# Kernel tuning notes

Hardware: AMD Instinct MI355X
Metric: run time of the kernel (lower is better)

Reference implementation:

```python
import jax, jax.numpy as jnp
import numpy as np

NUM_OBJ = 3
MIN_OBJ_SCALE = 0.1
MAX_OBJ_SCALE = 0.8
MIN_Y_SCALE = 0.75
MAX_Y_SCALE = 1.25
OBJ_POS_BOUND = 0.9
EPS_FIX = 0.095
BIG = 1e12


def setup_inputs() -> dict:
    key = jax.random.key(0)
    k1, k2, k3 = jax.random.split(key, 3)
    n, T, C, H, W = 64, 32, 3, 64, 64
    x = jax.random.normal(k1, (n, T, C, H, W), dtype=jnp.float32)
    d = C * H * W
    W_enc = jax.random.normal(k2, (d, NUM_OBJ * 8), dtype=jnp.float32) / np.sqrt(d).astype(np.float32)
    b_enc = jax.random.normal(k3, (NUM_OBJ * 8,), dtype=jnp.float32) * 0.01
    return {"x": x, "W_enc": W_enc, "b_enc": b_enc}


def _constrain_zp_mean(zp):
    # zp: (nTo, 8) -> mean (nTo, 4). std branch is discarded by forward().
    zm = jnp.concatenate([jax.nn.sigmoid(zp[:, 0:2]), 2.0 * jax.nn.sigmoid(zp[:, 2:4]) - 1.0], -1)
    set_max = jnp.array([[MAX_OBJ_SCALE - MIN_OBJ_SCALE, MAX_Y_SCALE - MIN_Y_SCALE, OBJ_POS_BOUND, OBJ_POS_BOUND]], dtype=zp.dtype)
    set_min = jnp.array([[MIN_OBJ_SCALE, MIN_Y_SCALE, 0.0, 0.0]], dtype=zp.dtype)
    return zm * set_max + set_min


def _greedy_assign(errors):
    # errors: (n, o, o). Greedy row-by-row argmin, masking out used columns with BIG,
    # exactly as the torch fault-fix loop does via scatter of 1e12.
    n, o, _ = errors.shape
    def step(used, i):
        e = errors[:, i, :] + used * BIG
        j = jnp.argmin(e, -1)
        used = used + jax.nn.one_hot(j, o, dtype=errors.dtype)
        return used, j
    _, js = jax.lax.scan(step, jnp.zeros((n, o), errors.dtype), jnp.arange(o))
    return jnp.moveaxis(js, 0, 1)  # (n, o)


def _match_objects(z):
    # z: (n, T, o, 4). Sequential greedy matching over time.
    def step(prev, z_t):
        curr = jax.lax.stop_gradient(z_t[:, :, 2:4])          # (n, o, 2)
        prv = jax.lax.stop_gradient(prev[:, :, 2:4])          # (n, o, 2)
        errors = jnp.sum((prv[:, :, None, :] - curr[:, None, :, :]) ** 2, -1)  # (n, i, j)
        idx = jnp.argmin(errors, -1)                          # (n, o)
        # fault = assignment is not a permutation (num_obj==3 check from source)
        ok = jnp.all(idx[:, 1:] != idx[:, :-1], -1) & (idx[:, 0] != idx[:, 2])
        gidx = _greedy_assign(errors)
        idx = jnp.where(ok[:, None], idx, gidx)
        match = jnp.take_along_axis(z_t, idx[:, :, None], axis=1)
        return match, match
    z0 = z[:, 0]
    _, rest = jax.lax.scan(step, z0, jnp.moveaxis(z[:, 1:], 1, 0))
    return jnp.concatenate([z0[:, None], jnp.moveaxis(rest, 0, 1)], 1)


def _fix_supair(z):
    # z: (n, T, o, 4). Replace isolated position jumps with neighbor average.
    n, T, o, d = z.shape
    diffs = jax.lax.stop_gradient(jnp.abs(z[:, 1:, :, :2] - z[:, :-1, :, :2]))
    zpad2 = jnp.zeros((n, 1, o, 2), z.dtype)
    prev = jnp.concatenate([zpad2, diffs], 1)
    after = jnp.concatenate([diffs, zpad2], 1)
    mask = (prev > EPS_FIX) & (after > EPS_FIX)               # (n, T, o, 2)
    zpad = jnp.zeros((n, 1, o, d), z.dtype)
    smooth = jnp.concatenate([zpad, (z[:, :-2] + z[:, 2:]) / 2, zpad], 1)
    mask_full = jnp.concatenate((d // 2) * [mask], -1)        # (n, T, o, 4)
    return jnp.where(mask_full, smooth, z)


def reference(x, W_enc, b_enc):
    n, T = x.shape[0], x.shape[1]
    # encoder: per-frame linear to (num_obj, 8) z-parameters
    zp = x.reshape(n * T, -1) @ W_enc + b_enc                  # (nT, o*8)
    zm = _constrain_zp_mean(zp.reshape(-1, 8))                 # (nTo, 4)
    z = zm.reshape(n, T, NUM_OBJ, 4)
    z = _match_objects(z)
    z = _fix_supair(z)
    # v_from_state
    v = z[:, 1:, :, 2:] - z[:, :-1, :, 2:]
    zf = jnp.concatenate([z[:, 1:], v], -1)                    # (n, T-1, o, 6)
    zf = jnp.concatenate([jnp.zeros_like(zf[:, 0:1]), zf], 1)  # (n, T, o, 6)
    zf = zf[:, 1:, :, 2:]                                      # (n, T-1, o, 4)
    zf = jnp.concatenate([(zf[..., :2] + 1) / 2 * 10, zf[..., 2:] / 2 * 10], -1)
    zf = jnp.concatenate([zf[..., :2] / 5, zf[..., 2:] * 2], -1)
    return zf
```

## Files before the change

kernel.cpp:

```cpp
#include <hip/hip_runtime.h>

#define N_B   64
#define T_S   32
#define DIM   12288
#define ROWS  2048
#define NCOL  12
#define RPB   16
#define KSPL  8
#define KSEG  (DIM / KSPL)
#define JSTEP (KSEG / 256)

__global__ __launch_bounds__(256) void k_tw(const float* __restrict__ W,
                                            float* __restrict__ Wt) {
    const int idx = blockIdx.x * 256 + threadIdx.x;
    const int c   = idx / DIM;
    const int k   = idx - c * DIM;
    const int cm  = ((c >> 2) << 3) | (c & 3);
    Wt[idx] = W[k * 24 + cm];
}

__global__ __launch_bounds__(256) void k_gemm(const float* __restrict__ x,
                                              const float* __restrict__ Wt,
                                              float* __restrict__ part) {
    const int rb   = blockIdx.x >> 3;
    const int sg   = blockIdx.x & 7;
    const int tid  = threadIdx.x;
    const int wave = tid >> 6;
    const int lane = tid & 63;
    const int r0   = rb * RPB + wave * 4;
    const int kb0  = sg * KSEG + lane * 4;

    float acc[4][NCOL];
#pragma unroll
    for (int r = 0; r < 4; ++r)
#pragma unroll
        for (int c = 0; c < NCOL; ++c) acc[r][c] = 0.f;

#pragma unroll 1
    for (int j = 0; j < JSTEP; ++j) {
        const int kb = kb0 + j * 256;
        float4 wv[NCOL];
#pragma unroll
        for (int c = 0; c < NCOL; ++c)
            wv[c] = *(const float4*)(Wt + (size_t)c * DIM + kb);
        float4 xv[4];
#pragma unroll
        for (int r = 0; r < 4; ++r)
            xv[r] = *(const float4*)(x + (size_t)(r0 + r) * DIM + kb);
#pragma unroll
        for (int r = 0; r < 4; ++r)
#pragma unroll
            for (int c = 0; c < NCOL; ++c)
                acc[r][c] += xv[r].x * wv[c].x + xv[r].y * wv[c].y +
                             xv[r].z * wv[c].z + xv[r].w * wv[c].w;
    }

#pragma unroll
    for (int r = 0; r < 4; ++r)
#pragma unroll
        for (int c = 0; c < NCOL; ++c) {
            float v = acc[r][c];
            v += __shfl_xor(v, 32, 64);
            v += __shfl_xor(v, 16, 64);
            v += __shfl_xor(v, 8, 64);
            v += __shfl_xor(v, 4, 64);
            v += __shfl_xor(v, 2, 64);
            v += __shfl_xor(v, 1, 64);
            acc[r][c] = v;
        }

    __shared__ float red[RPB * NCOL];
    if (lane == 0) {
#pragma unroll
        for (int r = 0; r < 4; ++r)
#pragma unroll
            for (int c = 0; c < NCOL; ++c)
                red[(wave * 4 + r) * NCOL + c] = acc[r][c];
    }
    __syncthreads();

    if (tid < RPB * NCOL)
        part[(size_t)sg * (ROWS * NCOL) + (size_t)rb * (RPB * NCOL) + tid] = red[tid];
}

__global__ __launch_bounds__(256) void k_reduce(const float* __restrict__ part,
                                                const float* __restrict__ b_enc,
                                                float* __restrict__ zbuf) {
    const int rc = blockIdx.x * 256 + threadIdx.x;
    float s = 0.f;
#pragma unroll
    for (int i = 0; i < KSPL; ++i) s += part[(size_t)i * (ROWS * NCOL) + rc];

    const int c  = rc % NCOL;
    const int o  = c >> 2;
    const int cp = c & 3;
    s += b_enc[o * 8 + cp];
    const float sg = 1.f / (1.f + expf(-s));
    float v;
    if (cp == 0)      v = sg * 0.7f + 0.1f;
    else if (cp == 1) v = sg * 0.5f + 0.75f;
    else              v = (2.f * sg - 1.f) * 0.9f;
    zbuf[rc] = v;
}

__global__ __launch_bounds__(64) void k_post(const float* __restrict__ zbuf,
                                             float* __restrict__ out) {
    __shared__ float z[T_S * NCOL];
    __shared__ float zm[T_S * NCOL];
    __shared__ float zf[T_S * NCOL];
    __shared__ int   perm[T_S];
    const int b   = blockIdx.x;
    const int tid = threadIdx.x;

#pragma unroll
    for (int i = 0; i < 6; ++i)
        z[tid + 64 * i] = zbuf[b * 384 + tid + 64 * i];
    __syncthreads();

    if (tid == 0) {
        float px0 = z[2],  py0 = z[3];
        float px1 = z[6],  py1 = z[7];
        float px2 = z[10], py2 = z[11];
        for (int t = 1; t < T_S; ++t) {
            const int base = t * 12;
            const float cx0 = z[base + 2],  cy0 = z[base + 3];
            const float cx1 = z[base + 6],  cy1 = z[base + 7];
            const float cx2 = z[base + 10], cy2 = z[base + 11];

            float dx, dy;
            dx = px0 - cx0; dy = py0 - cy0; const float e00 = dx * dx + dy * dy;
            dx = px0 - cx1; dy = py0 - cy1; const float e01 = dx * dx + dy * dy;
            dx = px0 - cx2; dy = py0 - cy2; const float e02 = dx * dx + dy * dy;
            dx = px1 - cx0; dy = py1 - cy0; const float e10 = dx * dx + dy * dy;
            dx = px1 - cx1; dy = py1 - cy1; const float e11 = dx * dx + dy * dy;
            dx = px1 - cx2; dy = py1 - cy2; const float e12 = dx * dx + dy * dy;
            dx = px2 - cx0; dy = py2 - cy0; const float e20 = dx * dx + dy * dy;
            dx = px2 - cx1; dy = py2 - cy1; const float e21 = dx * dx + dy * dy;
            dx = px2 - cx2; dy = py2 - cy2; const float e22 = dx * dx + dy * dy;

            auto amin3 = [](float a0, float a1, float a2) {
                int j = 0; float e = a0;
                if (a1 < e) { e = a1; j = 1; }
                if (a2 < e) { j = 2; }
                return j;
            };
            int i0 = amin3(e00, e01, e02);
            int i1 = amin3(e10, e11, e12);
            int i2 = amin3(e20, e21, e22);
            const bool ok = (i1 != i0) && (i2 != i1) && (i0 != i2);
            if (!ok) {
                float u0 = 0.f, u1 = 0.f, u2 = 0.f;
                i0 = amin3(e00, e01, e02);
                if (i0 == 0) u0 = 1.f; else if (i0 == 1) u1 = 1.f; else u2 = 1.f;
                i1 = amin3(e10 + u0 * 1e12f, e11 + u1 * 1e12f, e12 + u2 * 1e12f);
                if (i1 == 0) u0 = 1.f; else if (i1 == 1) u1 = 1.f; else u2 = 1.f;
                i2 = amin3(e20 + u0 * 1e12f, e21 + u1 * 1e12f, e22 + u2 * 1e12f);
            }
            perm[t] = i0 * 9 + i1 * 3 + i2;
            px0 = (i0 == 0) ? cx0 : (i0 == 1) ? cx1 : cx2;
            py0 = (i0 == 0) ? cy0 : (i0 == 1) ? cy1 : cy2;
            px1 = (i1 == 0) ? cx0 : (i1 == 1) ? cx1 : cx2;
            py1 = (i1 == 0) ? cy0 : (i1 == 1) ? cy1 : cy2;
            px2 = (i2 == 0) ? cx0 : (i2 == 1) ? cx1 : cx2;
            py2 = (i2 == 0) ? cy0 : (i2 == 1) ? cy1 : cy2;
        }
    }
    __syncthreads();

#pragma unroll
    for (int ii = 0; ii < 6; ++ii) {
        const int i  = tid + 64 * ii;
        const int t  = i / 12;
        const int j  = i - t * 12;
        const int k  = j >> 2;
        const int ch = j & 3;
        int p = k;
        if (t > 0) {
            const int code = perm[t];
            p = (k == 0) ? code / 9 : (k == 1) ? (code % 9) / 3 : code % 3;
        }
        zm[i] = z[t * 12 + p * 4 + ch];
    }
    __syncthreads();

#pragma unroll
    for (int ii = 0; ii < 6; ++ii) {
        const int i  = tid + 64 * ii;
        const int t  = i / 12;
        const int j  = i - t * 12;
        const int o  = j >> 2;
        const int cc = j & 1;
        const int mb = o * 4 + cc;
        const float pd = (t >= 1)  ? fabsf(zm[t * 12 + mb] - zm[(t - 1) * 12 + mb]) : 0.f;
        const float ad = (t <= 30) ? fabsf(zm[(t + 1) * 12 + mb] - zm[t * 12 + mb]) : 0.f;
        const bool  m  = (pd > 0.095f) && (ad > 0.095f);
        const float sm = (t >= 1 && t <= 30)
                             ? (zm[(t - 1) * 12 + j] + zm[(t + 1) * 12 + j]) * 0.5f
                             : 0.f;
        zf[i] = m ? sm : zm[t * 12 + j];
    }
    __syncthreads();

    for (int i = tid; i < 31 * 12; i += 64) {
        const int t  = i / 12;
        const int j  = i - t * 12;
        const int o  = j >> 2;
        const int c2 = j & 3;
        const int pb = o * 4 + 2 + (c2 & 1);
        float v;
        if (c2 < 2) v = zf[(t + 1) * 12 + pb] + 1.f;
        else        v = (zf[(t + 1) * 12 + pb] - zf[t * 12 + pb]) * 10.f;
        out[b * 372 + i] = v;
    }
}

extern "C" void kernel_launch(void* const* d_in, const int* in_sizes, int n_in,
                              void* d_out, int out_size, void* d_ws, size_t ws_size,
                              hipStream_t stream) {
    (void)in_sizes; (void)n_in; (void)out_size; (void)ws_size;
    const float* x     = (const float*)d_in[0];
    const float* W_enc = (const float*)d_in[1];
    const float* b_enc = (const float*)d_in[2];
    float* out  = (float*)d_out;

    float* zbuf = (float*)d_ws;
    float* Wt   = zbuf + ROWS * NCOL;
    float* part = Wt + NCOL * DIM;

    k_tw    <<<(NCOL * DIM) / 256, 256, 0, stream>>>(W_enc, Wt);
    k_gemm  <<<(ROWS / RPB) * KSPL, 256, 0, stream>>>(x, Wt, part);
    k_reduce<<<(ROWS * NCOL) / 256, 256, 0, stream>>>(part, b_enc, zbuf);
    k_post  <<<N_B, 64, 0, stream>>>(zbuf, out);
}
```

Baseline: 174.1 us.

## Double rows per wave in GEMM and split matching into a batch-parallel kernel

Each wave now handles 8 rows instead of 4, so every Wt load is reused across twice as many rows and the GEMM grid is halved. The greedy matching moves out of the single-thread-per-block post kernel into a dedicated kernel where one thread per batch runs the sequential scan over a time-major position buffer written by the reduce kernel. The greedy fallback is now computed branchlessly every step. This adds one more kernel launch and raises register pressure in the GEMM, which may lower occupancy.

```diff
diff --git a/kernel.cpp b/kernel.cpp
--- a/kernel.cpp
+++ b/kernel.cpp
@@ -5,7 +5,9 @@
 #define DIM   12288
 #define ROWS  2048
 #define NCOL  12
-#define RPB   16
+#define RPW   8
+#define WAVES 4
+#define RPB   (RPW * WAVES)
 #define KSPL  8
 #define KSEG  (DIM / KSPL)
 #define JSTEP (KSEG / 256)
@@ -27,36 +29,34 @@
     const int tid  = threadIdx.x;
     const int wave = tid >> 6;
     const int lane = tid & 63;
-    const int r0   = rb * RPB + wave * 4;
+    const int r0   = rb * RPB + wave * RPW;
     const int kb0  = sg * KSEG + lane * 4;
 
-    float acc[4][NCOL];
-#pragma unroll
-    for (int r = 0; r < 4; ++r)
+    float acc[RPW][NCOL];
+#pragma unroll
+    for (int r = 0; r < RPW; ++r)
 #pragma unroll
         for (int c = 0; c < NCOL; ++c) acc[r][c] = 0.f;
 
 #pragma unroll 1
     for (int j = 0; j < JSTEP; ++j) {
         const int kb = kb0 + j * 256;
-        float4 wv[NCOL];
-#pragma unroll
-        for (int c = 0; c < NCOL; ++c)
-            wv[c] = *(const float4*)(Wt + (size_t)c * DIM + kb);
-        float4 xv[4];
-#pragma unroll
-        for (int r = 0; r < 4; ++r)
+        float4 xv[RPW];
+#pragma unroll
+        for (int r = 0; r < RPW; ++r)
             xv[r] = *(const float4*)(x + (size_t)(r0 + r) * DIM + kb);
 #pragma unroll
-        for (int r = 0; r < 4; ++r)
-#pragma unroll
-            for (int c = 0; c < NCOL; ++c)
-                acc[r][c] += xv[r].x * wv[c].x + xv[r].y * wv[c].y +
-                             xv[r].z * wv[c].z + xv[r].w * wv[c].w;
-    }
-
-#pragma unroll
-    for (int r = 0; r < 4; ++r)
+        for (int c = 0; c < NCOL; ++c) {
+            const float4 wv = *(const float4*)(Wt + (size_t)c * DIM + kb);
+#pragma unroll
+            for (int r = 0; r < RPW; ++r)
+                acc[r][c] += xv[r].x * wv.x + xv[r].y * wv.y +
+                             xv[r].z * wv.z + xv[r].w * wv.w;
+        }
+    }
+
+#pragma unroll
+    for (int r = 0; r < RPW; ++r)
 #pragma unroll
         for (int c = 0; c < NCOL; ++c) {
             float v = acc[r][c];
@@ -72,28 +72,31 @@
     __shared__ float red[RPB * NCOL];
     if (lane == 0) {
 #pragma unroll
-        for (int r = 0; r < 4; ++r)
+        for (int r = 0; r < RPW; ++r)
 #pragma unroll
             for (int c = 0; c < NCOL; ++c)
-                red[(wave * 4 + r) * NCOL + c] = acc[r][c];
-    }
-    __syncthreads();
-
-    if (tid < RPB * NCOL)
-        part[(size_t)sg * (ROWS * NCOL) + (size_t)rb * (RPB * NCOL) + tid] = red[tid];
+                red[(wave * RPW + r) * NCOL + c] = acc[r][c];
+    }
+    __syncthreads();
+
+#pragma unroll
+    for (int i = tid; i < RPB * NCOL; i += 256)
+        part[(size_t)sg * (ROWS * NCOL) + (size_t)rb * (RPB * NCOL) + i] = red[i];
 }
 
 __global__ __launch_bounds__(256) void k_reduce(const float* __restrict__ part,
                                                 const float* __restrict__ b_enc,
-                                                float* __restrict__ zbuf) {
+                                                float* __restrict__ zbuf,
+                                                float* __restrict__ zmatch) {
     const int rc = blockIdx.x * 256 + threadIdx.x;
     float s = 0.f;
 #pragma unroll
     for (int i = 0; i < KSPL; ++i) s += part[(size_t)i * (ROWS * NCOL) + rc];
 
-    const int c  = rc % NCOL;
-    const int o  = c >> 2;
-    const int cp = c & 3;
+    const int row = rc / NCOL;
+    const int c   = rc - row * NCOL;
+    const int o   = c >> 2;
+    const int cp  = c & 3;
     s += b_enc[o * 8 + cp];
     const float sg = 1.f / (1.f + expf(-s));
     float v;
@@ -101,10 +104,75 @@
     else if (cp == 1) v = sg * 0.5f + 0.75f;
     else              v = (2.f * sg - 1.f) * 0.9f;
     zbuf[rc] = v;
-}
-
-__global__ __launch_bounds__(64) void k_post(const float* __restrict__ zbuf,
-                                             float* __restrict__ out) {
+
+    if (cp >= 2) {
+        const int b = row >> 5;
+        const int t = row & 31;
+        zmatch[((size_t)t * 64 + b) * 6 + o * 2 + (cp - 2)] = v;
+    }
+}
+
+__global__ __launch_bounds__(64) void k_match(const float* __restrict__ zmatch,
+                                              int* __restrict__ codes) {
+    const int b = threadIdx.x;
+
+    float px0 = zmatch[b * 6 + 0], py0 = zmatch[b * 6 + 1];
+    float px1 = zmatch[b * 6 + 2], py1 = zmatch[b * 6 + 3];
+    float px2 = zmatch[b * 6 + 4], py2 = zmatch[b * 6 + 5];
+
+    auto amin3 = [](float a0, float a1, float a2) {
+        int j = 0; float e = a0;
+        if (a1 < e) { e = a1; j = 1; }
+        if (a2 < e) { j = 2; }
+        return j;
+    };
+
+    for (int t = 1; t < T_S; ++t) {
+        const float* p = zmatch + ((size_t)t * 64 + b) * 6;
+        const float cx0 = p[0], cy0 = p[1];
+        const float cx1 = p[2], cy1 = p[3];
+        const float cx2 = p[4], cy2 = p[5];
+
+        float dx, dy;
+        dx = px0 - cx0; dy = py0 - cy0; const float e00 = dx * dx + dy * dy;
+        dx = px0 - cx1; dy = py0 - cy1; const float e01 = dx * dx + dy * dy;
+        dx = px0 - cx2; dy = py0 - cy2; const float e02 = dx * dx + dy * dy;
+        dx = px1 - cx0; dy = py1 - cy0; const float e10 = dx * dx + dy * dy;
+        dx = px1 - cx1; dy = py1 - cy1; const float e11 = dx * dx + dy * dy;
+        dx = px1 - cx2; dy = py1 - cy2; const float e12 = dx * dx + dy * dy;
+        dx = px2 - cx0; dy = py2 - cy0; const float e20 = dx * dx + dy * dy;
+        dx = px2 - cx1; dy = py2 - cy1; const float e21 = dx * dx + dy * dy;
+        dx = px2 - cx2; dy = py2 - cy2; const float e22 = dx * dx + dy * dy;
+
+        const int i0 = amin3(e00, e01, e02);
+        const int i1 = amin3(e10, e11, e12);
+        const int i2 = amin3(e20, e21, e22);
+
+        float u0 = (i0 == 0) ? 1e12f : 0.f;
+        float u1 = (i0 == 1) ? 1e12f : 0.f;
+        float u2 = (i0 == 2) ? 1e12f : 0.f;
+        const int g1 = amin3(e10 + u0, e11 + u1, e12 + u2);
+        if (g1 == 0) u0 = 1e12f; else if (g1 == 1) u1 = 1e12f; else u2 = 1e12f;
+        const int g2 = amin3(e20 + u0, e21 + u1, e22 + u2);
+
+        const bool ok = (i1 != i0) && (i2 != i1) && (i0 != i2);
+        const int f1 = ok ? i1 : g1;
+        const int f2 = ok ? i2 : g2;
+
+        codes[t * 64 + b] = i0 * 9 + f1 * 3 + f2;
+
+        px0 = (i0 == 0) ? cx0 : (i0 == 1) ? cx1 : cx2;
+        py0 = (i0 == 0) ? cy0 : (i0 == 1) ? cy1 : cy2;
+        px1 = (f1 == 0) ? cx0 : (f1 == 1) ? cx1 : cx2;
+        py1 = (f1 == 0) ? cy0 : (f1 == 1) ? cy1 : cy2;
+        px2 = (f2 == 0) ? cx0 : (f2 == 1) ? cx1 : cx2;
+        py2 = (f2 == 0) ? cy0 : (f2 == 1) ? cy1 : cy2;
+    }
+}
+
+__global__ __launch_bounds__(64) void k_apply(const float* __restrict__ zbuf,
+                                              const int* __restrict__ codes,
+                                              float* __restrict__ out) {
     __shared__ float z[T_S * NCOL];
     __shared__ float zm[T_S * NCOL];
     __shared__ float zf[T_S * NCOL];
@@ -115,56 +183,7 @@
 #pragma unroll
     for (int i = 0; i < 6; ++i)
         z[tid + 64 * i] = zbuf[b * 384 + tid + 64 * i];
-    __syncthreads();
-
-    if (tid == 0) {
-        float px0 = z[2],  py0 = z[3];
-        float px1 = z[6],  py1 = z[7];
-        float px2 = z[10], py2 = z[11];
-        for (int t = 1; t < T_S; ++t) {
-            const int base = t * 12;
-            const float cx0 = z[base + 2],  cy0 = z[base + 3];
-            const float cx1 = z[base + 6],  cy1 = z[base + 7];
-            const float cx2 = z[base + 10], cy2 = z[base + 11];
-
-            float dx, dy;
-            dx = px0 - cx0; dy = py0 - cy0; const float e00 = dx * dx + dy * dy;
-            dx = px0 - cx1; dy = py0 - cy1; const float e01 = dx * dx + dy * dy;
-            dx = px0 - cx2; dy = py0 - cy2; const float e02 = dx * dx + dy * dy;
-            dx = px1 - cx0; dy = py1 - cy0; const float e10 = dx * dx + dy * dy;
-            dx = px1 - cx1; dy = py1 - cy1; const float e11 = dx * dx + dy * dy;
-            dx = px1 - cx2; dy = py1 - cy2; const float e12 = dx * dx + dy * dy;
-            dx = px2 - cx0; dy = py2 - cy0; const float e20 = dx * dx + dy * dy;
-            dx = px2 - cx1; dy = py2 - cy1; const float e21 = dx * dx + dy * dy;
-            dx = px2 - cx2; dy = py2 - cy2; const float e22 = dx * dx + dy * dy;
-
-            auto amin3 = [](float a0, float a1, float a2) {
-                int j = 0; float e = a0;
-                if (a1 < e) { e = a1; j = 1; }
-                if (a2 < e) { j = 2; }
-                return j;
-            };
-            int i0 = amin3(e00, e01, e02);
-            int i1 = amin3(e10, e11, e12);
-            int i2 = amin3(e20, e21, e22);
-            const bool ok = (i1 != i0) && (i2 != i1) && (i0 != i2);
-            if (!ok) {
-                float u0 = 0.f, u1 = 0.f, u2 = 0.f;
-                i0 = amin3(e00, e01, e02);
-                if (i0 == 0) u0 = 1.f; else if (i0 == 1) u1 = 1.f; else u2 = 1.f;
-                i1 = amin3(e10 + u0 * 1e12f, e11 + u1 * 1e12f, e12 + u2 * 1e12f);
-                if (i1 == 0) u0 = 1.f; else if (i1 == 1) u1 = 1.f; else u2 = 1.f;
-                i2 = amin3(e20 + u0 * 1e12f, e21 + u1 * 1e12f, e22 + u2 * 1e12f);
-            }
-            perm[t] = i0 * 9 + i1 * 3 + i2;
-            px0 = (i0 == 0) ? cx0 : (i0 == 1) ? cx1 : cx2;
-            py0 = (i0 == 0) ? cy0 : (i0 == 1) ? cy1 : cy2;
-            px1 = (i1 == 0) ? cx0 : (i1 == 1) ? cx1 : cx2;
-            py1 = (i1 == 0) ? cy0 : (i1 == 1) ? cy1 : cy2;
-            px2 = (i2 == 0) ? cx0 : (i2 == 1) ? cx1 : cx2;
-            py2 = (i2 == 0) ? cy0 : (i2 == 1) ? cy1 : cy2;
-        }
-    }
+    if (tid >= 1 && tid < T_S) perm[tid] = codes[tid * 64 + b];
     __syncthreads();
 
 #pragma unroll
@@ -223,12 +242,15 @@
     const float* b_enc = (const float*)d_in[2];
     float* out  = (float*)d_out;
 
-    float* zbuf = (float*)d_ws;
-    float* Wt   = zbuf + ROWS * NCOL;
-    float* part = Wt + NCOL * DIM;
+    float* zbuf   = (float*)d_ws;
+    float* Wt     = zbuf + ROWS * NCOL;
+    float* part   = Wt + NCOL * DIM;
+    float* zmatch = part + KSPL * ROWS * NCOL;
+    int*   codes  = (int*)(zmatch + T_S * N_B * 6);
 
     k_tw    <<<(NCOL * DIM) / 256, 256, 0, stream>>>(W_enc, Wt);
     k_gemm  <<<(ROWS / RPB) * KSPL, 256, 0, stream>>>(x, Wt, part);
-    k_reduce<<<(ROWS * NCOL) / 256, 256, 0, stream>>>(part, b_enc, zbuf);
-    k_post  <<<N_B, 64, 0, stream>>>(zbuf, out);
-}
+    k_reduce<<<(ROWS * NCOL) / 256, 256, 0, stream>>>(part, b_enc, zbuf, zmatch);
+    k_match <<<1, 64, 0, stream>>>(zmatch, codes);
+    k_apply <<<N_B, 64, 0, stream>>>(zbuf, codes, out);
+}
```

Measured after the change: 190.6 us. 9.5% more time.

## Stage W slice in LDS per block, drop transpose kernel, raise K split

Applied to the files above, without the earlier changes.

Removes the separate W transpose kernel. Each GEMM block now loads and de-interleaves its K-segment of W_enc directly into shared memory. All x loads for the segment are issued up front before the barrier so they overlap with W staging. The K split grows from 8 to 16, doubling the number of blocks and the partial sums the reduce kernel reads. This saves a kernel launch and a global round trip, at the cost of 36KB of LDS per block and more registers for the preloaded x.

```diff
diff --git a/kernel.cpp b/kernel.cpp
--- a/kernel.cpp
+++ b/kernel.cpp
@@ -5,58 +5,68 @@
 #define DIM   12288
 #define ROWS  2048
 #define NCOL  12
-#define RPB   16
-#define KSPL  8
+#define RPW   4
+#define WAVES 4
+#define RPB   (RPW * WAVES)
+#define KSPL  16
 #define KSEG  (DIM / KSPL)
 #define JSTEP (KSEG / 256)
 
-__global__ __launch_bounds__(256) void k_tw(const float* __restrict__ W,
-                                            float* __restrict__ Wt) {
-    const int idx = blockIdx.x * 256 + threadIdx.x;
-    const int c   = idx / DIM;
-    const int k   = idx - c * DIM;
-    const int cm  = ((c >> 2) << 3) | (c & 3);
-    Wt[idx] = W[k * 24 + cm];
-}
-
 __global__ __launch_bounds__(256) void k_gemm(const float* __restrict__ x,
-                                              const float* __restrict__ Wt,
+                                              const float* __restrict__ W,
                                               float* __restrict__ part) {
-    const int rb   = blockIdx.x >> 3;
-    const int sg   = blockIdx.x & 7;
+    __shared__ float wt[NCOL * KSEG];
+    const int rb   = blockIdx.x >> 4;
+    const int sg   = blockIdx.x & 15;
     const int tid  = threadIdx.x;
     const int wave = tid >> 6;
     const int lane = tid & 63;
-    const int r0   = rb * RPB + wave * 4;
-    const int kb0  = sg * KSEG + lane * 4;
-
-    float acc[4][NCOL];
-#pragma unroll
-    for (int r = 0; r < 4; ++r)
+    const int r0   = rb * RPB + wave * RPW;
+    const int k00  = sg * KSEG;
+
+#pragma unroll
+    for (int it = 0; it < 9; ++it) {
+        const int flat = tid + it * 256;
+        const int k    = flat / 3;
+        const int g    = flat - 3 * k;
+        const float4 wv = *(const float4*)(W + (size_t)(k00 + k) * 24 + g * 8);
+        float* d = wt + (g * 4) * KSEG + k;
+        d[0 * KSEG] = wv.x;
+        d[1 * KSEG] = wv.y;
+        d[2 * KSEG] = wv.z;
+        d[3 * KSEG] = wv.w;
+    }
+
+    float4 xv[JSTEP][RPW];
+#pragma unroll
+    for (int j = 0; j < JSTEP; ++j)
+#pragma unroll
+        for (int r = 0; r < RPW; ++r)
+            xv[j][r] = *(const float4*)(x + (size_t)(r0 + r) * DIM + k00 + j * 256 + lane * 4);
+
+    __syncthreads();
+
+    float acc[RPW][NCOL];
+#pragma unroll
+    for (int r = 0; r < RPW; ++r)
 #pragma unroll
         for (int c = 0; c < NCOL; ++c) acc[r][c] = 0.f;
 
-#pragma unroll 1
+#pragma unroll
     for (int j = 0; j < JSTEP; ++j) {
-        const int kb = kb0 + j * 256;
-        float4 wv[NCOL];
-#pragma unroll
-        for (int c = 0; c < NCOL; ++c)
-            wv[c] = *(const float4*)(Wt + (size_t)c * DIM + kb);
-        float4 xv[4];
-#pragma unroll
-        for (int r = 0; r < 4; ++r)
-            xv[r] = *(const float4*)(x + (size_t)(r0 + r) * DIM + kb);
-#pragma unroll
-        for (int r = 0; r < 4; ++r)
-#pragma unroll
-            for (int c = 0; c < NCOL; ++c)
-                acc[r][c] += xv[r].x * wv[c].x + xv[r].y * wv[c].y +
-                             xv[r].z * wv[c].z + xv[r].w * wv[c].w;
-    }
-
-#pragma unroll
-    for (int r = 0; r < 4; ++r)
+        const int kl = j * 256 + lane * 4;
+#pragma unroll
+        for (int c = 0; c < NCOL; ++c) {
+            const float4 wv = *(const float4*)(wt + c * KSEG + kl);
+#pragma unroll
+            for (int r = 0; r < RPW; ++r)
+                acc[r][c] += xv[j][r].x * wv.x + xv[j][r].y * wv.y +
+                             xv[j][r].z * wv.z + xv[j][r].w * wv.w;
+        }
+    }
+
+#pragma unroll
+    for (int r = 0; r < RPW; ++r)
 #pragma unroll
         for (int c = 0; c < NCOL; ++c) {
             float v = acc[r][c];
@@ -69,13 +79,14 @@
             acc[r][c] = v;
         }
 
-    __shared__ float red[RPB * NCOL];
+    __syncthreads();
+    float* red = wt;
     if (lane == 0) {
 #pragma unroll
-        for (int r = 0; r < 4; ++r)
+        for (int r = 0; r < RPW; ++r)
 #pragma unroll
             for (int c = 0; c < NCOL; ++c)
-                red[(wave * 4 + r) * NCOL + c] = acc[r][c];
+                red[(wave * RPW + r) * NCOL + c] = acc[r][c];
     }
     __syncthreads();
 
@@ -91,9 +102,10 @@
 #pragma unroll
     for (int i = 0; i < KSPL; ++i) s += part[(size_t)i * (ROWS * NCOL) + rc];
 
-    const int c  = rc % NCOL;
-    const int o  = c >> 2;
-    const int cp = c & 3;
+    const int row = rc / NCOL;
+    const int c   = rc - row * NCOL;
+    const int o   = c >> 2;
+    const int cp  = c & 3;
     s += b_enc[o * 8 + cp];
     const float sg = 1.f / (1.f + expf(-s));
     float v;
@@ -224,11 +236,9 @@
     float* out  = (float*)d_out;
 
     float* zbuf = (float*)d_ws;
-    float* Wt   = zbuf + ROWS * NCOL;
-    float* part = Wt + NCOL * DIM;
-
-    k_tw    <<<(NCOL * DIM) / 256, 256, 0, stream>>>(W_enc, Wt);
-    k_gemm  <<<(ROWS / RPB) * KSPL, 256, 0, stream>>>(x, Wt, part);
+    float* part = zbuf + ROWS * NCOL;
+
+    k_gemm  <<<(ROWS / RPB) * KSPL, 256, 0, stream>>>(x, W_enc, part);
     k_reduce<<<(ROWS * NCOL) / 256, 256, 0, stream>>>(part, b_enc, zbuf);
     k_post  <<<N_B, 64, 0, stream>>>(zbuf, out);
 }
```

New measurement: 170.3 us. 1.02x faster.
